# Performance work log

Measured on AMD Instinct MI355X. Metric: run time of the kernel, lower is better.

Reference implementation:

```python
import jax, jax.numpy as jnp
import numpy as np

D_MODEL, HEAD, B, S = 1024, 64, 4, 2048

def setup_inputs() -> dict:
    key = jax.random.key(0)
    ks = jax.random.split(key, 7)
    sc = 0.02
    return {
        "x": jax.random.normal(ks[0], (B, S, D_MODEL), dtype=jnp.float32),
        "w_q": jax.random.normal(ks[1], (D_MODEL, HEAD), dtype=jnp.float32) * sc,
        "b_q": jax.random.normal(ks[2], (HEAD,), dtype=jnp.float32) * sc,
        "w_k": jax.random.normal(ks[3], (D_MODEL, HEAD), dtype=jnp.float32) * sc,
        "b_k": jax.random.normal(ks[4], (HEAD,), dtype=jnp.float32) * sc,
        "w_v": jax.random.normal(ks[5], (D_MODEL, HEAD), dtype=jnp.float32) * sc,
        "b_v": jax.random.normal(ks[6], (HEAD,), dtype=jnp.float32) * sc,
    }

def reference(x, w_q, b_q, w_k, b_k, w_v, b_v):
    # q, k, v: [B, S, H]
    q = jnp.einsum('bsd,dh->bsh', x, w_q) + b_q
    k = jnp.einsum('bsd,dh->bsh', x, w_k) + b_k
    v = jnp.einsum('bsd,dh->bsh', x, w_v) + b_v
    head = k.shape[-1]
    # Source divides by (1/sqrt(d)) i.e. multiplies by sqrt(d) -- kept faithful.
    scores = jnp.einsum('bqh,bkh->bqk', q, k) * jnp.sqrt(jnp.float32(head))
    seq = x.shape[1]
    causal = jnp.tril(jnp.ones((seq, seq), dtype=bool))  # [S, S]
    scores = jnp.where(causal, scores, -jnp.inf)
    att = jax.nn.softmax(scores, axis=-1)
    # dropout is identity in eval / p=0
    return jnp.einsum('bqk,bkh->bqh', att, v)
```

## Files before the change

kernel.cpp:

```cpp
#include <hip/hip_runtime.h>
#include <math.h>

#define D_MODEL 1024
#define HEAD 64
#define BATCH 4
#define SEQ 2048
#define M_TOT (BATCH*SEQ)

typedef short short8 __attribute__((ext_vector_type(8)));
typedef float f32x4 __attribute__((ext_vector_type(4)));
typedef unsigned short ushort_t;

__device__ __forceinline__ unsigned short f2bf(float x) {
    union { float f; unsigned u; } v; v.f = x;
    unsigned r = (v.u + 0x7FFFu + ((v.u >> 16) & 1u)) >> 16;
    return (unsigned short)r;
}
__device__ __forceinline__ unsigned short f2bf_trunc(float x) {
    union { float f; unsigned u; } v; v.f = x;
    return (unsigned short)(v.u >> 16);
}
__device__ __forceinline__ float bf2f(unsigned short h) {
    union { unsigned u; float f; } v; v.u = ((unsigned)h) << 16;
    return v.f;
}

__global__ __launch_bounds__(256) void wsplit_kernel(
    const float* __restrict__ wq, const float* __restrict__ wk,
    const float* __restrict__ wv,
    ushort_t* __restrict__ Wfhi, ushort_t* __restrict__ Wflo)
{
    int tid = blockIdx.x * 256 + threadIdx.x;
    int l = tid & 63;
    int c = l & 15, g = l >> 4;
    int rest = tid >> 6;
    int nt = rest % 12, ks = rest / 12;
    const float* W = (nt < 4) ? wq : ((nt < 8) ? wk : wv);
    int colm = ((nt & 3) * 16) + c;
    short8 hi, lo;
#pragma unroll
    for (int e = 0; e < 8; ++e) {
        float v = W[(size_t)(32 * ks + 8 * g + e) * HEAD + colm];
        unsigned short h = f2bf_trunc(v);
        hi[e] = (short)h;
        lo[e] = (short)f2bf(v - bf2f(h));
    }
    *(short8*)&Wfhi[(size_t)tid * 8] = hi;
    *(short8*)&Wflo[(size_t)tid * 8] = lo;
}

#define KSLAB 128
#define XSTR 132

__global__ __launch_bounds__(256) void proj_kernel(
    const float* __restrict__ x,
    const ushort_t* __restrict__ Wfhi, const ushort_t* __restrict__ Wflo,
    const float* __restrict__ bq, const float* __restrict__ bk,
    const float* __restrict__ bv,
    ushort_t* __restrict__ Qhi, ushort_t* __restrict__ Qlo,
    float* __restrict__ Kw, ushort_t* __restrict__ Vt)
{
    __shared__ __align__(16) ushort_t xh_lds[2][16][XSTR];
    __shared__ __align__(16) ushort_t xl_lds[2][16][XSTR];
    __shared__ float eld[4][3][16][17];

    const int t = threadIdx.x;
    const int w = t >> 6;
    const int l = t & 63;
    const int c = l & 15, g = l >> 4;
    const int m0 = blockIdx.x * 16;

    const int st_r = t >> 4;
    const int st_k = (t & 15) * 8;
    const float* xbase = &x[(size_t)(m0 + st_r) * D_MODEL + st_k];

    f32x4 acc[3];
#pragma unroll
    for (int j = 0; j < 3; ++j) acc[j] = (f32x4)0.0f;

    float4 ra, rb;
    {
        const float* xp = xbase;
        ra = *(const float4*)xp;
        rb = *(const float4*)(xp + 4);
    }
    {
        float xs[8] = {ra.x, ra.y, ra.z, ra.w, rb.x, rb.y, rb.z, rb.w};
        short8 hi, lo;
#pragma unroll
        for (int e = 0; e < 8; ++e) {
            unsigned short h = f2bf_trunc(xs[e]);
            hi[e] = (short)h;
            lo[e] = (short)f2bf(xs[e] - bf2f(h));
        }
        *(short8*)&xh_lds[0][st_r][st_k] = hi;
        *(short8*)&xl_lds[0][st_r][st_k] = lo;
    }

#pragma unroll 1
    for (int s = 0; s < 8; ++s) {
        __syncthreads();
        const int buf = s & 1;
        if (s < 7) {
            const float* xp = xbase + (s + 1) * KSLAB;
            ra = *(const float4*)xp;
            rb = *(const float4*)(xp + 4);
        }
#pragma unroll
        for (int ks = 0; ks < 4; ++ks) {
            short8 xh = *(const short8*)&xh_lds[buf][c][ks * 32 + 8 * g];
            short8 xl = *(const short8*)&xl_lds[buf][c][ks * 32 + 8 * g];
            const size_t kg = (size_t)(s * 4 + ks) * 6144;
#pragma unroll
            for (int j = 0; j < 3; ++j) {
                const size_t wo = kg + (size_t)((3 * w + j) * 64 + l) * 8;
                short8 wh = *(const short8*)&Wfhi[wo];
                short8 wl_ = *(const short8*)&Wflo[wo];
                acc[j] = __builtin_amdgcn_mfma_f32_16x16x32_bf16(xh, wh, acc[j], 0, 0, 0);
                acc[j] = __builtin_amdgcn_mfma_f32_16x16x32_bf16(xl, wh, acc[j], 0, 0, 0);
                acc[j] = __builtin_amdgcn_mfma_f32_16x16x32_bf16(xh, wl_, acc[j], 0, 0, 0);
            }
        }
        if (s < 7) {
            float xs[8] = {ra.x, ra.y, ra.z, ra.w, rb.x, rb.y, rb.z, rb.w};
            short8 hi, lo;
#pragma unroll
            for (int e = 0; e < 8; ++e) {
                unsigned short h = f2bf_trunc(xs[e]);
                hi[e] = (short)h;
                lo[e] = (short)f2bf(xs[e] - bf2f(h));
            }
            *(short8*)&xh_lds[buf ^ 1][st_r][st_k] = hi;
            *(short8*)&xl_lds[buf ^ 1][st_r][st_k] = lo;
        }
    }

#pragma unroll
    for (int j = 0; j < 3; ++j)
#pragma unroll
        for (int r = 0; r < 4; ++r)
            eld[w][j][4 * g + r][c] = acc[j][r];

    const int b = m0 >> 11;
    const int s0 = m0 & 2047;

#pragma unroll
    for (int j = 0; j < 3; ++j) {
        const int nt = 3 * w + j;
        const int col16 = (nt & 3) * 16;
        if (nt < 4) {
            const int row = l >> 2, cc4 = (l & 3) * 4;
            unsigned hu[2] = {0, 0}, lu[2] = {0, 0};
#pragma unroll
            for (int i = 0; i < 4; ++i) {
                float v = (eld[w][j][row][cc4 + i] + bq[col16 + cc4 + i]) * 8.0f;
                unsigned short h = f2bf_trunc(v);
                unsigned short lo2 = f2bf(v - bf2f(h));
                hu[i >> 1] |= ((unsigned)h) << ((i & 1) * 16);
                lu[i >> 1] |= ((unsigned)lo2) << ((i & 1) * 16);
            }
            size_t off = (size_t)(m0 + row) * HEAD + col16 + cc4;
            *(uint2*)&Qhi[off] = make_uint2(hu[0], hu[1]);
            *(uint2*)&Qlo[off] = make_uint2(lu[0], lu[1]);
        } else if (nt < 8) {
            const int row = l >> 2, cc4 = (l & 3) * 4;
            float4 o;
            o.x = eld[w][j][row][cc4 + 0] + bk[col16 + cc4 + 0];
            o.y = eld[w][j][row][cc4 + 1] + bk[col16 + cc4 + 1];
            o.z = eld[w][j][row][cc4 + 2] + bk[col16 + cc4 + 2];
            o.w = eld[w][j][row][cc4 + 3] + bk[col16 + cc4 + 3];
            *(float4*)&Kw[(size_t)(m0 + row) * HEAD + col16 + cc4] = o;
        } else {
            const int dl = l >> 2, sg = (l & 3) * 4;
            const float bb = bv[col16 + dl];
            unsigned vu[2] = {0, 0};
#pragma unroll
            for (int i = 0; i < 4; ++i) {
                unsigned short v = f2bf(eld[w][j][sg + i][dl] + bb);
                vu[i >> 1] |= ((unsigned)v) << ((i & 1) * 16);
            }
            *(uint2*)&Vt[((size_t)b * HEAD + col16 + dl) * SEQ + s0 + sg] =
                make_uint2(vu[0], vu[1]);
        }
    }
}

#define NW 8
#define CHUNK 16
#define PSTR 88

__global__ __launch_bounds__(512) void attn_kernel(
    const ushort_t* __restrict__ Qhi, const ushort_t* __restrict__ Qlo,
    const float* __restrict__ Kw,
    const ushort_t* __restrict__ Vt, float* __restrict__ out)
{
    __shared__ float Po[NW][CHUNK][68];
    __shared__ float Pm[NW][CHUNK];
    __shared__ float Pl[NW][CHUNK];
    __shared__ __align__(16) ushort_t Plds[NW][CHUNK][PSTR];

    const int t = threadIdx.x;
    const int w = t >> 6;
    const int l = t & 63;
    const int b = blockIdx.y;
    const int chunk = (int)gridDim.x - 1 - (int)blockIdx.x;
    const int q0 = chunk * CHUNK;
    const int c = l & 15;
    const int g = l >> 4;

    short8 qhi[2], qlo[2];
    {
        const ushort_t* qbase = &Qhi[(size_t)(b * SEQ + q0 + c) * HEAD];
        const ushort_t* qbasel = &Qlo[(size_t)(b * SEQ + q0 + c) * HEAD];
#pragma unroll
        for (int dc = 0; dc < 2; ++dc) {
            qhi[dc] = *(const short8*)&qbase[dc * 32 + 8 * g];
            qlo[dc] = *(const short8*)&qbasel[dc * 32 + 8 * g];
        }
    }

    f32x4 acc[4];
#pragma unroll
    for (int dt = 0; dt < 4; ++dt) acc[dt] = (f32x4)0.0f;
    float mrun = -1e30f, lsum = 0.f;

    const int ntiles = (q0 + CHUNK + 63) >> 6;
#pragma unroll 1
    for (int tile = w; tile < ntiles; tile += NW) {
        const int c0 = tile * 64;
        int nlive = ((q0 + 15 - c0) >> 4) + 1;
        nlive = nlive > 4 ? 4 : nlive;

        float sc[4][4];
        float pv[4][4];
#pragma unroll
        for (int t4 = 0; t4 < 4; ++t4)
#pragma unroll
            for (int r = 0; r < 4; ++r) pv[t4][r] = 0.f;

        float tmax = -1e30f;
#pragma unroll
        for (int t4 = 0; t4 < 4; ++t4) {
            if (t4 < nlive) {
                f32x4 st = (f32x4)0.0f;
#pragma unroll
                for (int dc = 0; dc < 2; ++dc) {
                    const float* kp = &Kw[(size_t)(b * SEQ + c0 + 16 * t4 + c) * HEAD + dc * 32 + 8 * g];
                    float4 a = *(const float4*)kp;
                    float4 b2 = *(const float4*)(kp + 4);
                    float ks8[8] = {a.x, a.y, a.z, a.w, b2.x, b2.y, b2.z, b2.w};
                    short8 khi, klo;
#pragma unroll
                    for (int e = 0; e < 8; ++e) {
                        unsigned short h = f2bf(ks8[e]);
                        khi[e] = (short)h;
                        klo[e] = (short)f2bf(ks8[e] - bf2f(h));
                    }
                    st = __builtin_amdgcn_mfma_f32_16x16x32_bf16(khi, qhi[dc], st, 0, 0, 0);
                    st = __builtin_amdgcn_mfma_f32_16x16x32_bf16(khi, qlo[dc], st, 0, 0, 0);
                    st = __builtin_amdgcn_mfma_f32_16x16x32_bf16(klo, qhi[dc], st, 0, 0, 0);
                }
#pragma unroll
                for (int r = 0; r < 4; ++r) {
                    int kv = c0 + 16 * t4 + 4 * g + r;
                    float s = (kv <= q0 + c) ? st[r] : -1e30f;
                    sc[t4][r] = s;
                    tmax = fmaxf(tmax, s);
                }
            }
        }
        tmax = fmaxf(tmax, __shfl_xor(tmax, 16));
        tmax = fmaxf(tmax, __shfl_xor(tmax, 32));
        float newm = fmaxf(mrun, tmax);
        float corr = __expf(mrun - newm);
        mrun = newm;

        float psum = 0.f;
#pragma unroll
        for (int t4 = 0; t4 < 4; ++t4) {
            if (t4 < nlive) {
#pragma unroll
                for (int r = 0; r < 4; ++r) {
                    float pp = __expf(sc[t4][r] - newm);
                    pv[t4][r] = pp;
                    psum += pp;
                }
            }
        }
        psum += __shfl_xor(psum, 16);
        psum += __shfl_xor(psum, 32);
        lsum = lsum * corr + psum;

#pragma unroll
        for (int r = 0; r < 4; ++r) {
            float cq = __shfl(corr, 4 * g + r);
#pragma unroll
            for (int dt = 0; dt < 4; ++dt) acc[dt][r] *= cq;
        }

#pragma unroll
        for (int t4 = 0; t4 < 4; ++t4) {
            uint2 u;
            u.x = (unsigned)f2bf(pv[t4][0]) | ((unsigned)f2bf(pv[t4][1]) << 16);
            u.y = (unsigned)f2bf(pv[t4][2]) | ((unsigned)f2bf(pv[t4][3]) << 16);
            *(uint2*)&Plds[w][c][16 * t4 + 4 * g] = u;
        }

        const int nkvc = (nlive + 1) >> 1;
#pragma unroll
        for (int kvc = 0; kvc < 2; ++kvc) {
            if (kvc < nkvc) {
                short8 pf = *(short8*)&Plds[w][c][kvc * 32 + 8 * g];
#pragma unroll
                for (int dt = 0; dt < 4; ++dt) {
                    const ushort_t* vp =
                        &Vt[((size_t)(b * HEAD) + 16 * dt + c) * SEQ + c0 + kvc * 32 + 8 * g];
                    short8 vf = *(const short8*)vp;
                    acc[dt] = __builtin_amdgcn_mfma_f32_16x16x32_bf16(pf, vf, acc[dt], 0, 0, 0);
                }
            }
        }
    }

    if (g == 0) { Pm[w][c] = mrun; Pl[w][c] = lsum; }
#pragma unroll
    for (int dt = 0; dt < 4; ++dt)
#pragma unroll
        for (int r = 0; r < 4; ++r)
            Po[w][4 * g + r][16 * dt + c] = acc[dt][r];
    __syncthreads();

    if (t < 256) {
        const int mr = t >> 4;
        const int md = (t & 15) * 4;
        float M = Pm[0][mr];
#pragma unroll
        for (int ww = 1; ww < NW; ++ww) M = fmaxf(M, Pm[ww][mr]);
        float L = 0.f;
        float4 O; O.x = O.y = O.z = O.w = 0.f;
#pragma unroll
        for (int ww = 0; ww < NW; ++ww) {
            float f = __expf(Pm[ww][mr] - M);
            L += f * Pl[ww][mr];
            float4 p = *(const float4*)&Po[ww][mr][md];
            O.x += f * p.x; O.y += f * p.y; O.z += f * p.z; O.w += f * p.w;
        }
        float inv = 1.0f / L;
        float4 res; res.x = O.x * inv; res.y = O.y * inv; res.z = O.z * inv; res.w = O.w * inv;
        *(float4*)&out[(size_t)(b * SEQ + q0 + mr) * HEAD + md] = res;
    }
}

extern "C" void kernel_launch(void* const* d_in, const int* in_sizes, int n_in,
                              void* d_out, int out_size, void* d_ws, size_t ws_size,
                              hipStream_t stream) {
    (void)in_sizes; (void)n_in; (void)out_size; (void)ws_size;
    const float* x  = (const float*)d_in[0];
    const float* wq = (const float*)d_in[1];
    const float* bq = (const float*)d_in[2];
    const float* wk = (const float*)d_in[3];
    const float* bk = (const float*)d_in[4];
    const float* wv = (const float*)d_in[5];
    const float* bv = (const float*)d_in[6];
    float* out = (float*)d_out;

    ushort_t* Wfhi = (ushort_t*)d_ws;
    ushort_t* Wflo = Wfhi + (size_t)D_MODEL * 192;
    ushort_t* Qhi  = Wflo + (size_t)D_MODEL * 192;
    ushort_t* Qlo  = Qhi + (size_t)M_TOT * HEAD;
    float*    Kw   = (float*)(Qlo + (size_t)M_TOT * HEAD);
    ushort_t* Vt   = (ushort_t*)(Kw + (size_t)M_TOT * HEAD);

    hipLaunchKernelGGL(wsplit_kernel, dim3(96), dim3(256), 0, stream,
                       wq, wk, wv, Wfhi, Wflo);
    hipLaunchKernelGGL(proj_kernel, dim3(M_TOT / 16), dim3(256), 0, stream,
                       x, Wfhi, Wflo, bq, bk, bv, Qhi, Qlo, Kw, Vt);
    hipLaunchKernelGGL(attn_kernel, dim3(SEQ / CHUNK, BATCH), dim3(512), 0, stream,
                       Qhi, Qlo, Kw, Vt, out);
}
```

Before: 89.86 us.

## Split attention over KV segments with separate merge kernel (split-K flash decoding)

```diff
diff --git a/kernel.cpp b/kernel.cpp
--- a/kernel.cpp
+++ b/kernel.cpp
@@ -185,14 +185,16 @@
     }
 }
 
-#define NW 8
+#define NW 4
 #define CHUNK 16
-#define PSTR 88
-
-__global__ __launch_bounds__(512) void attn_kernel(
+#define PSTR 72
+#define NSEG 4
+
+__global__ __launch_bounds__(256) void attn_part_kernel(
     const ushort_t* __restrict__ Qhi, const ushort_t* __restrict__ Qlo,
-    const float* __restrict__ Kw,
-    const ushort_t* __restrict__ Vt, float* __restrict__ out)
+    const float* __restrict__ Kw, const ushort_t* __restrict__ Vt,
+    float* __restrict__ Pm_ws, float* __restrict__ Pl_ws,
+    float* __restrict__ Po_ws)
 {
     __shared__ float Po[NW][CHUNK][68];
     __shared__ float Pm[NW][CHUNK];
@@ -202,9 +204,12 @@
     const int t = threadIdx.x;
     const int w = t >> 6;
     const int l = t & 63;
-    const int b = blockIdx.y;
-    const int chunk = (int)gridDim.x - 1 - (int)blockIdx.x;
+    const int chunk = blockIdx.x;
+    const int seg = blockIdx.y;
+    const int b = blockIdx.z;
     const int q0 = chunk * CHUNK;
+    if (seg * 512 > q0 + CHUNK - 1) return;
+
     const int c = l & 15;
     const int g = l >> 4;
 
@@ -224,20 +229,16 @@
     for (int dt = 0; dt < 4; ++dt) acc[dt] = (f32x4)0.0f;
     float mrun = -1e30f, lsum = 0.f;
 
-    const int ntiles = (q0 + CHUNK + 63) >> 6;
 #pragma unroll 1
-    for (int tile = w; tile < ntiles; tile += NW) {
-        const int c0 = tile * 64;
+    for (int i = 0; i < 2; ++i) {
+        const int tl = seg * 8 + w + 4 * i;
+        const int c0 = tl * 64;
+        if (c0 > q0 + CHUNK - 1) continue;
+
         int nlive = ((q0 + 15 - c0) >> 4) + 1;
         nlive = nlive > 4 ? 4 : nlive;
 
         float sc[4][4];
-        float pv[4][4];
-#pragma unroll
-        for (int t4 = 0; t4 < 4; ++t4)
-#pragma unroll
-            for (int r = 0; r < 4; ++r) pv[t4][r] = 0.f;
-
         float tmax = -1e30f;
 #pragma unroll
         for (int t4 = 0; t4 < 4; ++t4) {
@@ -267,6 +268,9 @@
                     sc[t4][r] = s;
                     tmax = fmaxf(tmax, s);
                 }
+            } else {
+#pragma unroll
+                for (int r = 0; r < 4; ++r) sc[t4][r] = -1e30f;
             }
         }
         tmax = fmaxf(tmax, __shfl_xor(tmax, 16));
@@ -282,9 +286,12 @@
 #pragma unroll
                 for (int r = 0; r < 4; ++r) {
                     float pp = __expf(sc[t4][r] - newm);
-                    pv[t4][r] = pp;
+                    sc[t4][r] = pp;
                     psum += pp;
                 }
+            } else {
+#pragma unroll
+                for (int r = 0; r < 4; ++r) sc[t4][r] = 0.f;
             }
         }
         psum += __shfl_xor(psum, 16);
@@ -301,11 +308,10 @@
 #pragma unroll
         for (int t4 = 0; t4 < 4; ++t4) {
             uint2 u;
-            u.x = (unsigned)f2bf(pv[t4][0]) | ((unsigned)f2bf(pv[t4][1]) << 16);
-            u.y = (unsigned)f2bf(pv[t4][2]) | ((unsigned)f2bf(pv[t4][3]) << 16);
+            u.x = (unsigned)f2bf(sc[t4][0]) | ((unsigned)f2bf(sc[t4][1]) << 16);
+            u.y = (unsigned)f2bf(sc[t4][2]) | ((unsigned)f2bf(sc[t4][3]) << 16);
             *(uint2*)&Plds[w][c][16 * t4 + 4 * g] = u;
         }
-
         const int nkvc = (nlive + 1) >> 1;
 #pragma unroll
         for (int kvc = 0; kvc < 2; ++kvc) {
@@ -330,25 +336,56 @@
             Po[w][4 * g + r][16 * dt + c] = acc[dt][r];
     __syncthreads();
 
-    if (t < 256) {
-        const int mr = t >> 4;
-        const int md = (t & 15) * 4;
-        float M = Pm[0][mr];
-#pragma unroll
-        for (int ww = 1; ww < NW; ++ww) M = fmaxf(M, Pm[ww][mr]);
-        float L = 0.f;
-        float4 O; O.x = O.y = O.z = O.w = 0.f;
-#pragma unroll
-        for (int ww = 0; ww < NW; ++ww) {
-            float f = __expf(Pm[ww][mr] - M);
-            L += f * Pl[ww][mr];
-            float4 p = *(const float4*)&Po[ww][mr][md];
-            O.x += f * p.x; O.y += f * p.y; O.z += f * p.z; O.w += f * p.w;
-        }
-        float inv = 1.0f / L;
-        float4 res; res.x = O.x * inv; res.y = O.y * inv; res.z = O.z * inv; res.w = O.w * inv;
-        *(float4*)&out[(size_t)(b * SEQ + q0 + mr) * HEAD + md] = res;
-    }
+    const int mr = t >> 4;
+    const int md = (t & 15) * 4;
+    float M = Pm[0][mr];
+#pragma unroll
+    for (int ww = 1; ww < NW; ++ww) M = fmaxf(M, Pm[ww][mr]);
+    float L = 0.f;
+    float4 O; O.x = O.y = O.z = O.w = 0.f;
+#pragma unroll
+    for (int ww = 0; ww < NW; ++ww) {
+        float f = __expf(Pm[ww][mr] - M);
+        L += f * Pl[ww][mr];
+        float4 p = *(const float4*)&Po[ww][mr][md];
+        O.x += f * p.x; O.y += f * p.y; O.z += f * p.z; O.w += f * p.w;
+    }
+    const size_t part = ((size_t)(b * 128 + chunk)) * NSEG + seg;
+    *(float4*)&Po_ws[(part * CHUNK + mr) * HEAD + md] = O;
+    if ((t & 15) == 0) {
+        Pm_ws[part * CHUNK + mr] = M;
+        Pl_ws[part * CHUNK + mr] = L;
+    }
+}
+
+__global__ __launch_bounds__(256) void attn_merge_kernel(
+    const float* __restrict__ Pm_ws, const float* __restrict__ Pl_ws,
+    const float* __restrict__ Po_ws, float* __restrict__ out)
+{
+    const int t = threadIdx.x;
+    const int chunk = blockIdx.x;
+    const int b = blockIdx.y;
+    const int nparts = (chunk >> 5) + 1;
+    const int mr = t >> 4;
+    const int md = (t & 15) * 4;
+    const size_t pbase = ((size_t)(b * 128 + chunk)) * NSEG;
+
+    float M = -1e30f;
+#pragma unroll 1
+    for (int p = 0; p < nparts; ++p)
+        M = fmaxf(M, Pm_ws[(pbase + p) * CHUNK + mr]);
+    float L = 0.f;
+    float4 O; O.x = O.y = O.z = O.w = 0.f;
+#pragma unroll 1
+    for (int p = 0; p < nparts; ++p) {
+        float f = __expf(Pm_ws[(pbase + p) * CHUNK + mr] - M);
+        L += f * Pl_ws[(pbase + p) * CHUNK + mr];
+        float4 po = *(const float4*)&Po_ws[((pbase + p) * CHUNK + mr) * HEAD + md];
+        O.x += f * po.x; O.y += f * po.y; O.z += f * po.z; O.w += f * po.w;
+    }
+    float inv = 1.0f / L;
+    float4 res; res.x = O.x * inv; res.y = O.y * inv; res.z = O.z * inv; res.w = O.w * inv;
+    *(float4*)&out[(size_t)(b * SEQ + chunk * CHUNK + mr) * HEAD + md] = res;
 }
 
 extern "C" void kernel_launch(void* const* d_in, const int* in_sizes, int n_in,
@@ -370,11 +407,16 @@
     ushort_t* Qlo  = Qhi + (size_t)M_TOT * HEAD;
     float*    Kw   = (float*)(Qlo + (size_t)M_TOT * HEAD);
     ushort_t* Vt   = (ushort_t*)(Kw + (size_t)M_TOT * HEAD);
+    float* Pm_ws = (float*)(Vt + (size_t)M_TOT * HEAD);
+    float* Pl_ws = Pm_ws + (size_t)BATCH * 128 * NSEG * CHUNK;
+    float* Po_ws = Pl_ws + (size_t)BATCH * 128 * NSEG * CHUNK;
 
     hipLaunchKernelGGL(wsplit_kernel, dim3(96), dim3(256), 0, stream,
                        wq, wk, wv, Wfhi, Wflo);
     hipLaunchKernelGGL(proj_kernel, dim3(M_TOT / 16), dim3(256), 0, stream,
                        x, Wfhi, Wflo, bq, bk, bv, Qhi, Qlo, Kw, Vt);
-    hipLaunchKernelGGL(attn_kernel, dim3(SEQ / CHUNK, BATCH), dim3(512), 0, stream,
-                       Qhi, Qlo, Kw, Vt, out);
-}
+    hipLaunchKernelGGL(attn_part_kernel, dim3(SEQ / CHUNK, NSEG, BATCH), dim3(256),
+                       0, stream, Qhi, Qlo, Kw, Vt, Pm_ws, Pl_ws, Po_ws);
+    hipLaunchKernelGGL(attn_merge_kernel, dim3(SEQ / CHUNK, BATCH), dim3(256),
+                       0, stream, Pm_ws, Pl_ws, Po_ws, out);
+}
```

Result: faster. 82.66 us (-8.0%).
